# Optimization experiments

Measured on AMD Instinct MI355X. Metric: run time of the kernel, lower is better.

## Reference

```python
import jax, jax.numpy as jnp
import numpy as np

N_NODES = 80000
N_EDGES = 1280000
IN_CH = 128
OUT_CH = 32
HID = 2 * OUT_CH


def gcn_conv(x, W, b, src, dst, n_nodes):
    """PyG GCNConv with self-loops and symmetric normalization.
    out[i] = b + sum_{j->i} deg(j)^-1/2 deg(i)^-1/2 (x_j @ W)
    """
    loop = jnp.arange(n_nodes, dtype=src.dtype)
    s = jnp.concatenate([src, loop])  # [E+N]
    d = jnp.concatenate([dst, loop])  # [E+N]
    deg = jax.ops.segment_sum(jnp.ones_like(d, dtype=x.dtype), d,
                              num_segments=n_nodes)  # in-degree incl. self loop
    dinv = jnp.where(deg > 0, jax.lax.rsqrt(deg), 0.0)
    norm = dinv[s] * dinv[d]  # [E+N]
    h = x @ W  # [N, F_out] dense transform first (fewer flops when F_out < F_in)
    msg = h[s] * norm[:, None]  # [E+N, F_out] gather + scale
    out = jax.ops.segment_sum(msg, d, num_segments=n_nodes)  # scatter-add
    return out + b


def setup_inputs() -> dict:
    key = jax.random.key(0)
    k1, k2, k3, k4 = jax.random.split(key, 4)
    x = jax.random.normal(k1, (N_NODES, IN_CH), dtype=jnp.float32)
    edge_index = jax.random.randint(k2, (2, N_EDGES), 0, N_NODES, dtype=jnp.int64)
    W1 = jax.random.normal(k3, (IN_CH, HID), dtype=jnp.float32) / np.sqrt(IN_CH)
    b1 = jnp.zeros((HID,), dtype=jnp.float32)
    W2 = jax.random.normal(k4, (HID, OUT_CH), dtype=jnp.float32) / np.sqrt(HID)
    b2 = jnp.zeros((OUT_CH,), dtype=jnp.float32)
    return {"x": x, "edge_index": edge_index, "W1": W1, "b1": b1,
            "W2": W2, "b2": b2}


def reference(x, edge_index, W1, b1, W2, b2):
    src, dst = edge_index[0], edge_index[1]
    h = jax.nn.relu(gcn_conv(x, W1, b1, src, dst, N_NODES))
    return gcn_conv(h, W2, b2, src, dst, N_NODES)
```

## Files before the change

### kernel.cpp

```cpp
#include <hip/hip_runtime.h>
#include <hip/hip_fp16.h>

#define N_NODES 80000
#define N_EDGES 1280000
#define IN_CH 128
#define HID 64
#define OUT_CH 32

#define NBUCK 625
#define CAP 3072
#define BIN_BLOCKS 128
#define ELLW 24

typedef float vf2 __attribute__((ext_vector_type(2)));
typedef float vf4 __attribute__((ext_vector_type(4)));
typedef short short8 __attribute__((ext_vector_type(8)));
typedef float floatx4 __attribute__((ext_vector_type(4)));

__device__ __forceinline__ unsigned bf16rn(float x) {
    unsigned u = __float_as_uint(x);
    return (u + 0x7FFFu + ((u >> 16) & 1u)) >> 16;
}
__device__ __forceinline__ unsigned packbf2(float a, float b) {
    return bf16rn(a) | (bf16rn(b) << 16);
}
__device__ __forceinline__ float hl(unsigned u) {
    return __half2float(__ushort_as_half((unsigned short)(u & 0xFFFFu)));
}
__device__ __forceinline__ float hh(unsigned u) {
    return __half2float(__ushort_as_half((unsigned short)(u >> 16)));
}
__device__ __forceinline__ unsigned pack2h(float a, float b) {
    return (unsigned)__half_as_ushort(__float2half_rn(a)) |
           ((unsigned)__half_as_ushort(__float2half_rn(b)) << 16);
}

__global__ __launch_bounds__(512, 6) void k_bin_gemm1(
        const int* __restrict__ src, const int* __restrict__ dst,
        int* __restrict__ gcur, unsigned int* __restrict__ binned,
        const float* __restrict__ x, const float* __restrict__ W1,
        unsigned short* __restrict__ h1h) {
    __shared__ unsigned short smem_u[26112];
    int bid = blockIdx.x, t = threadIdx.x;
    if (bid < BIN_BLOCKS) {
        int* hist = (int*)smem_u;
        int* lcur = hist + NBUCK;
        const int chunk = N_EDGES / BIN_BLOCKS;
        int e0 = bid * chunk;
        int e1 = e0 + chunk;
        for (int i = t; i < NBUCK; i += 512) hist[i] = 0;
        __syncthreads();
        for (int e = e0 + t; e < e1; e += 512)
            atomicAdd(&hist[dst[e] >> 7], 1);
        __syncthreads();
        for (int i = t; i < NBUCK; i += 512) {
            int h = hist[i];
            lcur[i] = h ? atomicAdd(&gcur[i], h) : 0;
        }
        __syncthreads();
        for (int e = e0 + t; e < e1; e += 512) {
            int d = dst[e];
            int bk = d >> 7;
            int pos = atomicAdd(&lcur[bk], 1);
            if (pos < CAP)
                binned[(size_t)bk * CAP + pos] =
                    (unsigned int)src[e] | ((unsigned int)(d & 127) << 17);
        }
    } else {
        unsigned short* sX = smem_u;
        unsigned short* sWT = smem_u + 128 * 136;
        long long nb = (long long)(bid - BIN_BLOCKS) * 128;
        if (bid == BIN_BLOCKS && t < 16)
            *(uint2*)&h1h[(size_t)N_NODES * 64 + t * 4] = (uint2){0u, 0u};
        for (int it = 0; it < 8; ++it) {
            int idx = t + it * 512;
            int node = idx >> 5, k4 = (idx & 31) * 4;
            float4 v = *(const float4*)&x[(nb + node) * IN_CH + k4];
            unsigned u0 = packbf2(v.x, v.y), u1 = packbf2(v.z, v.w);
            *(uint2*)&sX[node * 136 + k4] = (uint2){u0, u1};
        }
        for (int it = 0; it < 4; ++it) {
            int idx = t + it * 512;
            int k = idx >> 4, c4 = (idx & 15) * 4;
            float4 w = *(const float4*)&W1[k * 64 + c4];
            sWT[(c4 + 0) * 136 + k] = (unsigned short)bf16rn(w.x);
            sWT[(c4 + 1) * 136 + k] = (unsigned short)bf16rn(w.y);
            sWT[(c4 + 2) * 136 + k] = (unsigned short)bf16rn(w.z);
            sWT[(c4 + 3) * 136 + k] = (unsigned short)bf16rn(w.w);
        }
        __syncthreads();
        int wv = t >> 6, lane = t & 63;
        int lm = lane & 15, q = lane >> 4;
        int m0 = wv * 16;
        floatx4 acc[4];
#pragma unroll
        for (int j = 0; j < 4; ++j) acc[j] = (floatx4){0.f, 0.f, 0.f, 0.f};
#pragma unroll
        for (int kk = 0; kk < 128; kk += 32) {
            short8 a0 = *(short8*)&sX[(m0 + lm) * 136 + kk + q * 8];
#pragma unroll
            for (int ct = 0; ct < 4; ++ct) {
                short8 bfr = *(short8*)&sWT[(ct * 16 + lm) * 136 + kk + q * 8];
                acc[ct] = __builtin_amdgcn_mfma_f32_16x16x32_bf16(a0, bfr, acc[ct], 0, 0, 0);
            }
        }
#pragma unroll
        for (int ct = 0; ct < 4; ++ct)
#pragma unroll
            for (int r = 0; r < 4; ++r) {
                long long node = nb + m0 + q * 4 + r;
                int c = ct * 16 + lm;
                h1h[node * 64 + c] = __half_as_ushort(__float2half_rn(acc[ct][r]));
            }
    }
}

__global__ __launch_bounds__(256) void k_csr(const unsigned int* __restrict__ binned,
                                             const int* __restrict__ cnt,
                                             int* __restrict__ csr,
                                             int* __restrict__ ell,
                                             int2* __restrict__ rse,
                                             float2* __restrict__ meta,
                                             unsigned int* __restrict__ h1u,
                                             unsigned int* __restrict__ g2u) {
    __shared__ int deg[128];
    __shared__ int scan[128];
    __shared__ int cur[128];
    __shared__ int rst[128];
    __shared__ float sdinv[128];
    int bk = blockIdx.x, t = threadIdx.x;
    int n_e = min(cnt[bk], CAP);
    const unsigned int* eb = binned + (size_t)bk * CAP;
    if (bk == 0 && t < 16) g2u[(size_t)N_NODES * 16 + t] = 0u;
    if (t < 128) deg[t] = 0;
    __syncthreads();
    for (int i = t; i < n_e; i += 256) atomicAdd(&deg[eb[i] >> 17], 1);
    __syncthreads();
    if (t < 128) scan[t] = deg[t];
    __syncthreads();
    for (int off = 1; off < 128; off <<= 1) {
        int v = (t < 128 && t >= off) ? scan[t - off] : 0;
        __syncthreads();
        if (t < 128) scan[t] += v;
        __syncthreads();
    }
    if (t < 128) {
        int incl = scan[t];
        int s = incl - deg[t];
        cur[t] = s;
        rst[t] = s;
        int n = bk * 128 + t;
        int base = bk * CAP;
        rse[n] = make_int2(base + s, base + incl);
        float dv = rsqrtf((float)(deg[t] + 1));
        meta[n] = make_float2(dv, (float)deg[t]);
        sdinv[t] = dv;
    }
    int* eb_ell = ell + (size_t)bk * 128 * ELLW;
    for (int i = t; i < 128 * ELLW; i += 256) eb_ell[i] = N_NODES;
    __syncthreads();
    for (int i = t; i < n_e; i += 256) {
        unsigned int p = eb[i];
        int dL = p >> 17;
        int pos = atomicAdd(&cur[dL], 1);
        int s = (int)(p & 0x1FFFF);
        csr[bk * CAP + pos] = s;
        int lp = pos - rst[dL];
        if (lp < ELLW) eb_ell[dL * ELLW + lp] = s;
    }
    size_t rbase = (size_t)bk * 128 * 32;
    for (int i = t; i < 128 * 16; i += 256) {
        int row = i >> 4, c = i & 15;
        uint2 u = *(uint2*)&h1u[rbase + (size_t)row * 32 + 2 * c];
        float dv = sdinv[row];
        u.x = pack2h(dv * hl(u.x), dv * hh(u.x));
        u.y = pack2h(dv * hl(u.y), dv * hh(u.y));
        *(uint2*)&h1u[rbase + (size_t)row * 32 + 2 * c] = u;
    }
}

__global__ __launch_bounds__(256) void k_agg64(
        const unsigned int* __restrict__ h1u, const int* __restrict__ ell,
        const int* __restrict__ csr, const int2* __restrict__ rse,
        const float2* __restrict__ meta, const float* __restrict__ b1,
        const float* __restrict__ W2, unsigned int* __restrict__ g2u) {
    __shared__ float sW2[64 * 32];
    __shared__ float sH2[4][2][64];
    int t = threadIdx.x;
    for (int i = t * 2; i < 64 * 32; i += 512)
        *(vf2*)&sW2[i] = *(const vf2*)&W2[i];

    int wv = t >> 6, lane = t & 63;
    int nd = lane >> 5;
    int q  = (lane >> 4) & 1;
    int fo = lane & 15;
    int col = lane & 31;
    int n = blockIdx.x * 8 + wv * 2 + nd;

    float2 mt = meta[n];
    float dn = mt.x;
    int dg = (int)mt.y;
    uint2 un = *(const uint2*)&h1u[(size_t)n * 32 + 2 * fo];
    float4 bb = *(const float4*)&b1[4 * fo];
    const int* er = ell + (size_t)n * ELLW;
    int4 w0 = *(const int4*)&er[0];
    int4 w1 = *(const int4*)&er[4];
    int4 w2 = *(const int4*)&er[8];
    int4 w3 = *(const int4*)&er[12];
    int4 w4 = *(const int4*)&er[16];
    int4 w5 = *(const int4*)&er[20];
    int ss[12];
    ss[0]  = q ? w0.y : w0.x;  ss[1]  = q ? w0.w : w0.z;
    ss[2]  = q ? w1.y : w1.x;  ss[3]  = q ? w1.w : w1.z;
    ss[4]  = q ? w2.y : w2.x;  ss[5]  = q ? w2.w : w2.z;
    ss[6]  = q ? w3.y : w3.x;  ss[7]  = q ? w3.w : w3.z;
    ss[8]  = q ? w4.y : w4.x;  ss[9]  = q ? w4.w : w4.z;
    ss[10] = q ? w5.y : w5.x;  ss[11] = q ? w5.w : w5.z;
    float ax = 0.f, ay = 0.f, az = 0.f, aw = 0.f;
#pragma unroll
    for (int i = 0; i < 12; ++i) {
        uint2 u = *(const uint2*)&h1u[(size_t)ss[i] * 32 + 2 * fo];
        ax += hl(u.x); ay += hh(u.x); az += hl(u.y); aw += hh(u.y);
    }
    if (dg > ELLW) {
        int2 rb = rse[n];
        for (int e = rb.x + ELLW + q; e < rb.y; e += 2) {
            int s = csr[e];
            uint2 u = *(const uint2*)&h1u[(size_t)s * 32 + 2 * fo];
            ax += hl(u.x); ay += hh(u.x); az += hl(u.y); aw += hh(u.y);
        }
    }
    ax += __shfl_down(ax, 16); ay += __shfl_down(ay, 16);
    az += __shfl_down(az, 16); aw += __shfl_down(aw, 16);
    __syncthreads();
    if (q == 0) {
        ax += hl(un.x); ay += hh(un.x); az += hl(un.y); aw += hh(un.y);
        vf4 h2v = {fmaxf(dn * ax + bb.x, 0.f), fmaxf(dn * ay + bb.y, 0.f),
                   fmaxf(dn * az + bb.z, 0.f), fmaxf(dn * aw + bb.w, 0.f)};
        *(vf4*)&sH2[wv][nd][4 * fo] = h2v;
    }
    __syncthreads();
    int nd2 = lane >> 5;
    const float* hrow = sH2[wv][nd2];
    float g = 0.f;
#pragma unroll
    for (int k = 0; k < 64; ++k) g += hrow[k] * sW2[k * 32 + col];
    g *= dn;
    float g1 = __shfl_down(g, 1);
    float g2v = __shfl_down(g, 2);
    float g3v = __shfl_down(g, 3);
    if ((lane & 3) == 0) {
        uint2 p = {pack2h(g, g1), pack2h(g2v, g3v)};
        *(uint2*)&g2u[(size_t)n * 16 + (col >> 1)] = p;
    }
}

__global__ __launch_bounds__(256) void k_agg32(
        const unsigned int* __restrict__ g2u, const int* __restrict__ ell,
        const int* __restrict__ csr, const int2* __restrict__ rse,
        const float2* __restrict__ meta, const float* __restrict__ b2,
        float* __restrict__ outp) {
    int n = blockIdx.x * 4 + (threadIdx.x >> 6);
    int lane = threadIdx.x & 63;
    int oc = lane >> 3, fo = lane & 7;
    float2 mt = meta[n];
    float dn = mt.x;
    int dg = (int)mt.y;
    uint2 un = *(const uint2*)&g2u[(size_t)n * 16 + 2 * fo];
    const int* er = ell + (size_t)n * ELLW;
    int s0 = er[oc];
    int s1 = er[oc + 8];
    int s2 = er[oc + 16];
    uint2 u0 = *(const uint2*)&g2u[(size_t)s0 * 16 + 2 * fo];
    uint2 u1 = *(const uint2*)&g2u[(size_t)s1 * 16 + 2 * fo];
    uint2 u2 = *(const uint2*)&g2u[(size_t)s2 * 16 + 2 * fo];
    float ax, ay, az, aw;
    ax  = hl(u0.x); ay  = hh(u0.x); az  = hl(u0.y); aw  = hh(u0.y);
    ax += hl(u1.x); ay += hh(u1.x); az += hl(u1.y); aw += hh(u1.y);
    ax += hl(u2.x); ay += hh(u2.x); az += hl(u2.y); aw += hh(u2.y);
    if (dg > ELLW) {
        int2 rb = rse[n];
        for (int e = rb.x + ELLW + oc; e < rb.y; e += 8) {
            int s = csr[e];
            uint2 u = *(const uint2*)&g2u[(size_t)s * 16 + 2 * fo];
            ax += hl(u.x); ay += hh(u.x); az += hl(u.y); aw += hh(u.y);
        }
    }
    ax += __shfl_down(ax, 32); ay += __shfl_down(ay, 32);
    az += __shfl_down(az, 32); aw += __shfl_down(aw, 32);
    ax += __shfl_down(ax, 16); ay += __shfl_down(ay, 16);
    az += __shfl_down(az, 16); aw += __shfl_down(aw, 16);
    ax += __shfl_down(ax, 8);  ay += __shfl_down(ay, 8);
    az += __shfl_down(az, 8);  aw += __shfl_down(aw, 8);
    if (oc == 0) {
        ax += hl(un.x); ay += hh(un.x);
        az += hl(un.y); aw += hh(un.y);
        float4 bbv = *(const float4*)&b2[4 * fo];
        vf4 o = {dn * ax + bbv.x, dn * ay + bbv.y, dn * az + bbv.z, dn * aw + bbv.w};
        __builtin_nontemporal_store(o, (vf4*)&outp[(size_t)n * 32 + 4 * fo]);
    }
}

static inline size_t align256(size_t x) { return (x + 255) & ~(size_t)255; }

extern "C" void kernel_launch(void* const* d_in, const int* in_sizes, int n_in,
                              void* d_out, int out_size, void* d_ws, size_t ws_size,
                              hipStream_t stream) {
    const float* x  = (const float*)d_in[0];
    const int*   ei = (const int*)d_in[1];
    const float* W1 = (const float*)d_in[2];
    const float* b1 = (const float*)d_in[3];
    const float* W2 = (const float*)d_in[4];
    const float* b2 = (const float*)d_in[5];
    float* out = (float*)d_out;

    const int* src = ei;
    const int* dst = ei + N_EDGES;

    char* ws = (char*)d_ws;
    size_t off = 0;
    int* gcur = (int*)(ws + off);              off = align256(off + NBUCK * 4);
    unsigned int* binned = (unsigned int*)(ws + off);
                                               off = align256(off + (size_t)NBUCK * CAP * 4);
    int* csr = (int*)(ws + off);               off = align256(off + (size_t)NBUCK * CAP * 4);
    int* ell = (int*)(ws + off);               off = align256(off + (size_t)N_NODES * ELLW * 4);
    int2* rse = (int2*)(ws + off);             off = align256(off + (size_t)N_NODES * 8);
    float2* meta = (float2*)(ws + off);        off = align256(off + (size_t)N_NODES * 8);
    unsigned short* h1h = (unsigned short*)(ws + off);
                                               off = align256(off + (size_t)(N_NODES + 1) * 64 * 2);
    unsigned int* g2u = (unsigned int*)(ws + off);
                                               off = align256(off + (size_t)(N_NODES + 1) * 16 * 4);

    (void)hipMemsetAsync(gcur, 0, NBUCK * 4, stream);
    k_bin_gemm1<<<BIN_BLOCKS + N_NODES / 128, 512, 0, stream>>>(src, dst, gcur, binned,
                                                                x, W1, h1h);
    k_csr<<<NBUCK, 256, 0, stream>>>(binned, gcur, csr, ell, rse, meta,
                                     (unsigned int*)h1h, g2u);
    k_agg64<<<N_NODES / 8, 256, 0, stream>>>((const unsigned int*)h1h, ell, csr, rse,
                                             meta, b1, W2, g2u);
    k_agg32<<<N_NODES / 4, 256, 0, stream>>>(g2u, ell, csr, rse, meta, b2, out);
}
```

Measured before the change: 194.2 us.

## Replace bucketed CSR build with direct global-atomic ELL fill plus overflow list

Drops the two-pass bucket binning and per-bucket CSR kernel. Edges now go straight into a fixed-width ELL table (width raised to 32) by taking one global atomic counter slot per destination node. Edges beyond the width go into a small global overflow list, which overflowing nodes scan linearly. Degree normalization and prescaling move into a light per-node k_meta kernel, and empty ELL slots are marked 0xFF by memset and clamped to the zero sentinel row. This removes a kernel and a round trip over the binned edges, but adds heavy contention on global atomics, extra gathers for padded slots, and a linear overflow scan whose cost could be large.

```diff
diff --git a/kernel.cpp b/kernel.cpp
--- a/kernel.cpp
+++ b/kernel.cpp
@@ -7,10 +7,9 @@
 #define HID 64
 #define OUT_CH 32
 
-#define NBUCK 625
-#define CAP 3072
-#define BIN_BLOCKS 128
-#define ELLW 24
+#define BIN_BLOCKS 125
+#define ELLW 32
+#define OVF_CAP 8192
 
 typedef float vf2 __attribute__((ext_vector_type(2)));
 typedef float vf4 __attribute__((ext_vector_type(4)));
@@ -34,37 +33,41 @@
     return (unsigned)__half_as_ushort(__float2half_rn(a)) |
            ((unsigned)__half_as_ushort(__float2half_rn(b)) << 16);
 }
+__device__ __forceinline__ int clampid(int s) {
+    unsigned v = (unsigned)s;
+    return (int)(v > (unsigned)N_NODES ? (unsigned)N_NODES : v);
+}
 
 __global__ __launch_bounds__(512, 6) void k_bin_gemm1(
         const int* __restrict__ src, const int* __restrict__ dst,
-        int* __restrict__ gcur, unsigned int* __restrict__ binned,
+        int* __restrict__ cnt, int* __restrict__ ell,
+        int2* __restrict__ ovf, int* __restrict__ ovfcnt,
         const float* __restrict__ x, const float* __restrict__ W1,
         unsigned short* __restrict__ h1h) {
     __shared__ unsigned short smem_u[26112];
     int bid = blockIdx.x, t = threadIdx.x;
     if (bid < BIN_BLOCKS) {
-        int* hist = (int*)smem_u;
-        int* lcur = hist + NBUCK;
         const int chunk = N_EDGES / BIN_BLOCKS;
         int e0 = bid * chunk;
         int e1 = e0 + chunk;
-        for (int i = t; i < NBUCK; i += 512) hist[i] = 0;
-        __syncthreads();
-        for (int e = e0 + t; e < e1; e += 512)
-            atomicAdd(&hist[dst[e] >> 7], 1);
-        __syncthreads();
-        for (int i = t; i < NBUCK; i += 512) {
-            int h = hist[i];
-            lcur[i] = h ? atomicAdd(&gcur[i], h) : 0;
-        }
-        __syncthreads();
-        for (int e = e0 + t; e < e1; e += 512) {
-            int d = dst[e];
-            int bk = d >> 7;
-            int pos = atomicAdd(&lcur[bk], 1);
-            if (pos < CAP)
-                binned[(size_t)bk * CAP + pos] =
-                    (unsigned int)src[e] | ((unsigned int)(d & 127) << 17);
+        for (int base = e0 + t; base < e1; base += 2048) {
+            int d[4], s[4], p[4];
+#pragma unroll
+            for (int k = 0; k < 4; ++k) {
+                d[k] = dst[base + k * 512];
+                s[k] = src[base + k * 512];
+            }
+#pragma unroll
+            for (int k = 0; k < 4; ++k) p[k] = atomicAdd(&cnt[d[k]], 1);
+#pragma unroll
+            for (int k = 0; k < 4; ++k) {
+                if (p[k] < ELLW) {
+                    ell[(size_t)d[k] * ELLW + p[k]] = s[k];
+                } else {
+                    int o = atomicAdd(ovfcnt, 1);
+                    if (o < OVF_CAP) ovf[o] = make_int2(d[k], s[k]);
+                }
+            }
         }
     } else {
         unsigned short* sX = smem_u;
@@ -115,73 +118,25 @@
     }
 }
 
-__global__ __launch_bounds__(256) void k_csr(const unsigned int* __restrict__ binned,
-                                             const int* __restrict__ cnt,
-                                             int* __restrict__ csr,
-                                             int* __restrict__ ell,
-                                             int2* __restrict__ rse,
-                                             float2* __restrict__ meta,
-                                             unsigned int* __restrict__ h1u,
-                                             unsigned int* __restrict__ g2u) {
-    __shared__ int deg[128];
-    __shared__ int scan[128];
-    __shared__ int cur[128];
-    __shared__ int rst[128];
-    __shared__ float sdinv[128];
-    int bk = blockIdx.x, t = threadIdx.x;
-    int n_e = min(cnt[bk], CAP);
-    const unsigned int* eb = binned + (size_t)bk * CAP;
-    if (bk == 0 && t < 16) g2u[(size_t)N_NODES * 16 + t] = 0u;
-    if (t < 128) deg[t] = 0;
-    __syncthreads();
-    for (int i = t; i < n_e; i += 256) atomicAdd(&deg[eb[i] >> 17], 1);
-    __syncthreads();
-    if (t < 128) scan[t] = deg[t];
-    __syncthreads();
-    for (int off = 1; off < 128; off <<= 1) {
-        int v = (t < 128 && t >= off) ? scan[t - off] : 0;
-        __syncthreads();
-        if (t < 128) scan[t] += v;
-        __syncthreads();
-    }
-    if (t < 128) {
-        int incl = scan[t];
-        int s = incl - deg[t];
-        cur[t] = s;
-        rst[t] = s;
-        int n = bk * 128 + t;
-        int base = bk * CAP;
-        rse[n] = make_int2(base + s, base + incl);
-        float dv = rsqrtf((float)(deg[t] + 1));
-        meta[n] = make_float2(dv, (float)deg[t]);
-        sdinv[t] = dv;
-    }
-    int* eb_ell = ell + (size_t)bk * 128 * ELLW;
-    for (int i = t; i < 128 * ELLW; i += 256) eb_ell[i] = N_NODES;
-    __syncthreads();
-    for (int i = t; i < n_e; i += 256) {
-        unsigned int p = eb[i];
-        int dL = p >> 17;
-        int pos = atomicAdd(&cur[dL], 1);
-        int s = (int)(p & 0x1FFFF);
-        csr[bk * CAP + pos] = s;
-        int lp = pos - rst[dL];
-        if (lp < ELLW) eb_ell[dL * ELLW + lp] = s;
-    }
-    size_t rbase = (size_t)bk * 128 * 32;
-    for (int i = t; i < 128 * 16; i += 256) {
-        int row = i >> 4, c = i & 15;
-        uint2 u = *(uint2*)&h1u[rbase + (size_t)row * 32 + 2 * c];
-        float dv = sdinv[row];
-        u.x = pack2h(dv * hl(u.x), dv * hh(u.x));
-        u.y = pack2h(dv * hl(u.y), dv * hh(u.y));
-        *(uint2*)&h1u[rbase + (size_t)row * 32 + 2 * c] = u;
-    }
+__global__ __launch_bounds__(256) void k_meta(
+        const int* __restrict__ cnt, float2* __restrict__ meta,
+        unsigned int* __restrict__ h1u, unsigned int* __restrict__ g2u) {
+    int gid = blockIdx.x * 256 + threadIdx.x;
+    int n = gid >> 4, c = gid & 15;
+    if (blockIdx.x == 0 && threadIdx.x < 16)
+        g2u[(size_t)N_NODES * 16 + threadIdx.x] = 0u;
+    int dg = cnt[n];
+    float dv = rsqrtf((float)(dg + 1));
+    if (c == 0) meta[n] = make_float2(dv, (float)dg);
+    uint2 u = *(uint2*)&h1u[(size_t)n * 32 + 2 * c];
+    u.x = pack2h(dv * hl(u.x), dv * hh(u.x));
+    u.y = pack2h(dv * hl(u.y), dv * hh(u.y));
+    *(uint2*)&h1u[(size_t)n * 32 + 2 * c] = u;
 }
 
 __global__ __launch_bounds__(256) void k_agg64(
         const unsigned int* __restrict__ h1u, const int* __restrict__ ell,
-        const int* __restrict__ csr, const int2* __restrict__ rse,
+        const int2* __restrict__ ovf, const int* __restrict__ ovfcnt,
         const float2* __restrict__ meta, const float* __restrict__ b1,
         const float* __restrict__ W2, unsigned int* __restrict__ g2u) {
     __shared__ float sW2[64 * 32];
@@ -209,31 +164,38 @@
     int4 w3 = *(const int4*)&er[12];
     int4 w4 = *(const int4*)&er[16];
     int4 w5 = *(const int4*)&er[20];
-    int ss[12];
+    int4 w6 = *(const int4*)&er[24];
+    int4 w7 = *(const int4*)&er[28];
+    int ss[16];
     ss[0]  = q ? w0.y : w0.x;  ss[1]  = q ? w0.w : w0.z;
     ss[2]  = q ? w1.y : w1.x;  ss[3]  = q ? w1.w : w1.z;
     ss[4]  = q ? w2.y : w2.x;  ss[5]  = q ? w2.w : w2.z;
     ss[6]  = q ? w3.y : w3.x;  ss[7]  = q ? w3.w : w3.z;
     ss[8]  = q ? w4.y : w4.x;  ss[9]  = q ? w4.w : w4.z;
     ss[10] = q ? w5.y : w5.x;  ss[11] = q ? w5.w : w5.z;
+    ss[12] = q ? w6.y : w6.x;  ss[13] = q ? w6.w : w6.z;
+    ss[14] = q ? w7.y : w7.x;  ss[15] = q ? w7.w : w7.z;
     float ax = 0.f, ay = 0.f, az = 0.f, aw = 0.f;
 #pragma unroll
-    for (int i = 0; i < 12; ++i) {
-        uint2 u = *(const uint2*)&h1u[(size_t)ss[i] * 32 + 2 * fo];
+    for (int i = 0; i < 16; ++i) {
+        int s = clampid(ss[i]);
+        uint2 u = *(const uint2*)&h1u[(size_t)s * 32 + 2 * fo];
         ax += hl(u.x); ay += hh(u.x); az += hl(u.y); aw += hh(u.y);
-    }
-    if (dg > ELLW) {
-        int2 rb = rse[n];
-        for (int e = rb.x + ELLW + q; e < rb.y; e += 2) {
-            int s = csr[e];
-            uint2 u = *(const uint2*)&h1u[(size_t)s * 32 + 2 * fo];
-            ax += hl(u.x); ay += hh(u.x); az += hl(u.y); aw += hh(u.y);
-        }
     }
     ax += __shfl_down(ax, 16); ay += __shfl_down(ay, 16);
     az += __shfl_down(az, 16); aw += __shfl_down(aw, 16);
     __syncthreads();
     if (q == 0) {
+        if (dg > ELLW) {
+            int m = min(ovfcnt[0], OVF_CAP);
+            for (int i = 0; i < m; ++i) {
+                int2 oe = ovf[i];
+                if (oe.x == n) {
+                    uint2 u = *(const uint2*)&h1u[(size_t)oe.y * 32 + 2 * fo];
+                    ax += hl(u.x); ay += hh(u.x); az += hl(u.y); aw += hh(u.y);
+                }
+            }
+        }
         ax += hl(un.x); ay += hh(un.x); az += hl(un.y); aw += hh(un.y);
         vf4 h2v = {fmaxf(dn * ax + bb.x, 0.f), fmaxf(dn * ay + bb.y, 0.f),
                    fmaxf(dn * az + bb.z, 0.f), fmaxf(dn * aw + bb.w, 0.f)};
@@ -257,7 +219,7 @@
 
 __global__ __launch_bounds__(256) void k_agg32(
         const unsigned int* __restrict__ g2u, const int* __restrict__ ell,
-        const int* __restrict__ csr, const int2* __restrict__ rse,
+        const int2* __restrict__ ovf, const int* __restrict__ ovfcnt,
         const float2* __restrict__ meta, const float* __restrict__ b2,
         float* __restrict__ outp) {
     int n = blockIdx.x * 4 + (threadIdx.x >> 6);
@@ -268,24 +230,19 @@
     int dg = (int)mt.y;
     uint2 un = *(const uint2*)&g2u[(size_t)n * 16 + 2 * fo];
     const int* er = ell + (size_t)n * ELLW;
-    int s0 = er[oc];
-    int s1 = er[oc + 8];
-    int s2 = er[oc + 16];
+    int s0 = clampid(er[oc]);
+    int s1 = clampid(er[oc + 8]);
+    int s2 = clampid(er[oc + 16]);
+    int s3 = clampid(er[oc + 24]);
     uint2 u0 = *(const uint2*)&g2u[(size_t)s0 * 16 + 2 * fo];
     uint2 u1 = *(const uint2*)&g2u[(size_t)s1 * 16 + 2 * fo];
     uint2 u2 = *(const uint2*)&g2u[(size_t)s2 * 16 + 2 * fo];
+    uint2 u3 = *(const uint2*)&g2u[(size_t)s3 * 16 + 2 * fo];
     float ax, ay, az, aw;
     ax  = hl(u0.x); ay  = hh(u0.x); az  = hl(u0.y); aw  = hh(u0.y);
     ax += hl(u1.x); ay += hh(u1.x); az += hl(u1.y); aw += hh(u1.y);
     ax += hl(u2.x); ay += hh(u2.x); az += hl(u2.y); aw += hh(u2.y);
-    if (dg > ELLW) {
-        int2 rb = rse[n];
-        for (int e = rb.x + ELLW + oc; e < rb.y; e += 8) {
-            int s = csr[e];
-            uint2 u = *(const uint2*)&g2u[(size_t)s * 16 + 2 * fo];
-            ax += hl(u.x); ay += hh(u.x); az += hl(u.y); aw += hh(u.y);
-        }
-    }
+    ax += hl(u3.x); ay += hh(u3.x); az += hl(u3.y); aw += hh(u3.y);
     ax += __shfl_down(ax, 32); ay += __shfl_down(ay, 32);
     az += __shfl_down(az, 32); aw += __shfl_down(aw, 32);
     ax += __shfl_down(ax, 16); ay += __shfl_down(ay, 16);
@@ -293,6 +250,16 @@
     ax += __shfl_down(ax, 8);  ay += __shfl_down(ay, 8);
     az += __shfl_down(az, 8);  aw += __shfl_down(aw, 8);
     if (oc == 0) {
+        if (dg > ELLW) {
+            int m = min(ovfcnt[0], OVF_CAP);
+            for (int i = 0; i < m; ++i) {
+                int2 oe = ovf[i];
+                if (oe.x == n) {
+                    uint2 u = *(const uint2*)&g2u[(size_t)oe.y * 16 + 2 * fo];
+                    ax += hl(u.x); ay += hh(u.x); az += hl(u.y); aw += hh(u.y);
+                }
+            }
+        }
         ax += hl(un.x); ay += hh(un.x);
         az += hl(un.y); aw += hh(un.y);
         float4 bbv = *(const float4*)&b2[4 * fo];
@@ -319,24 +286,22 @@
 
     char* ws = (char*)d_ws;
     size_t off = 0;
-    int* gcur = (int*)(ws + off);              off = align256(off + NBUCK * 4);
-    unsigned int* binned = (unsigned int*)(ws + off);
-                                               off = align256(off + (size_t)NBUCK * CAP * 4);
-    int* csr = (int*)(ws + off);               off = align256(off + (size_t)NBUCK * CAP * 4);
+    int* cnt = (int*)(ws + off);               off = align256(off + (size_t)(N_NODES + 64) * 4);
+    int* ovfcnt = cnt + N_NODES;
+    int2* ovf = (int2*)(ws + off);             off = align256(off + (size_t)OVF_CAP * 8);
     int* ell = (int*)(ws + off);               off = align256(off + (size_t)N_NODES * ELLW * 4);
-    int2* rse = (int2*)(ws + off);             off = align256(off + (size_t)N_NODES * 8);
     float2* meta = (float2*)(ws + off);        off = align256(off + (size_t)N_NODES * 8);
     unsigned short* h1h = (unsigned short*)(ws + off);
                                                off = align256(off + (size_t)(N_NODES + 1) * 64 * 2);
     unsigned int* g2u = (unsigned int*)(ws + off);
                                                off = align256(off + (size_t)(N_NODES + 1) * 16 * 4);
 
-    (void)hipMemsetAsync(gcur, 0, NBUCK * 4, stream);
-    k_bin_gemm1<<<BIN_BLOCKS + N_NODES / 128, 512, 0, stream>>>(src, dst, gcur, binned,
-                                                                x, W1, h1h);
-    k_csr<<<NBUCK, 256, 0, stream>>>(binned, gcur, csr, ell, rse, meta,
-                                     (unsigned int*)h1h, g2u);
-    k_agg64<<<N_NODES / 8, 256, 0, stream>>>((const unsigned int*)h1h, ell, csr, rse,
+    (void)hipMemsetAsync(cnt, 0, (size_t)(N_NODES + 64) * 4, stream);
+    (void)hipMemsetAsync(ell, 0xFF, (size_t)N_NODES * ELLW * 4, stream);
+    k_bin_gemm1<<<BIN_BLOCKS + N_NODES / 128, 512, 0, stream>>>(src, dst, cnt, ell,
+                                                                ovf, ovfcnt, x, W1, h1h);
+    k_meta<<<N_NODES * 16 / 256, 256, 0, stream>>>(cnt, meta, (unsigned int*)h1h, g2u);
+    k_agg64<<<N_NODES / 8, 256, 0, stream>>>((const unsigned int*)h1h, ell, ovf, ovfcnt,
                                              meta, b1, W2, g2u);
-    k_agg32<<<N_NODES / 4, 256, 0, stream>>>(g2u, ell, csr, rse, meta, b2, out);
-}
+    k_agg32<<<N_NODES / 4, 256, 0, stream>>>(g2u, ell, ovf, ovfcnt, meta, b2, out);
+}
```

Result: slower. 238.7 us (+22.9%).
